# Performance work log

Hardware: AMD Instinct MI355X
Metric: run time of the kernel (lower is better)

Reference implementation:

```python
import jax, jax.numpy as jnp
import numpy as np

EPS = 1e-12  # torch F.normalize eps


def unfold(x, ksize, pad):
    # torch F.unfold equivalent: [B,C,H,W] -> [B, C*k*k, L], channel-major ordering
    patches = jax.lax.conv_general_dilated_patches(
        x, (ksize, ksize), (1, 1), [(pad, pad), (pad, pad)],
        dimension_numbers=('NCHW', 'OIHW', 'NCHW'))
    B, CKK, Hp, Wp = patches.shape
    return patches.reshape(B, CKK, Hp * Wp)


def fold(patches, C, ksize, H, W, pad):
    # torch F.fold equivalent (stride 1): overlap-add of [B, C*k*k, H*W] -> [B,C,H,W]
    B = patches.shape[0]
    p = patches.reshape(B, C, ksize, ksize, H, W)
    out = jnp.zeros((B, C, H + 2 * pad, W + 2 * pad), patches.dtype)
    for di in range(ksize):
        for dj in range(ksize):
            out = out.at[:, :, di:di + H, dj:dj + W].add(p[:, :, di, dj])
    return out[:, :, pad:pad + H, pad:pad + W]


def setup_inputs() -> dict:
    key = jax.random.key(0)
    ks = jax.random.split(key, 4)
    B, C, H, W = 2, 512, 64, 64
    D, CIN = 256, 512 * 9  # embed: Linear(tdim*8*3*3 -> tdim*4), tdim=64
    return {
        'query': jax.random.normal(ks[0], (B, C, H, W), dtype=jnp.float32),
        'key': jax.random.normal(ks[1], (B, C, H, W), dtype=jnp.float32),
        'value': jax.random.normal(ks[2], (B, C, H, W), dtype=jnp.float32),
        'W_embed': jax.random.normal(ks[3], (D, CIN), dtype=jnp.float32) * 0.02,
        'k': 3,
    }


def reference(query, key, value, W_embed, k):
    B, Cv, H, W = value.shape
    # patch embed: unfold -> linear (no bias)
    q_unf = unfold(query, k, k // 2)                       # [B, C*k*k, L]
    k_unf = unfold(key, k, k // 2)                         # [B, C*k*k, L]
    k_emb = jnp.einsum('bcl,dc->bld', k_unf, W_embed)      # [B, L, D]
    q_emb = jnp.einsum('bcl,dc->bdl', q_unf, W_embed)      # [B, D, L]
    # cosine correlation
    k_n = k_emb / jnp.maximum(jnp.linalg.norm(k_emb, axis=2, keepdims=True), EPS)
    q_n = q_emb / jnp.maximum(jnp.linalg.norm(q_emb, axis=1, keepdims=True), EPS)
    corr = jnp.einsum('bld,bdm->blm', k_n, q_n)            # [B, L_key, L_query]
    corr_value = jnp.max(corr, axis=1)                     # [B, L]
    corr_argmax = jnp.argmax(corr, axis=1)                 # [B, L]
    # swap(V=value, idx=corr_argmax, s=1, k=k)
    s = 1
    temph = s * k + H * s - H - s                          # = k - 1
    tempw = s * k + W * s - W - s
    ph = max(temph // 2 + temph % 2, 1)
    pw = max(tempw // 2 + tempw % 2, 1)
    v_unf = unfold(value, k, ph)                           # [B, Cv*k*k, L] (ph==pw for square)
    t_unf = jnp.take_along_axis(v_unf, corr_argmax[:, None, :], axis=2)
    divisor = fold(jnp.ones_like(t_unf), Cv, k, H, W, ph)
    T = fold(t_unf, Cv, k, H, W, ph) / divisor             # [B, Cv, H, W]
    S = corr_value.reshape(B, 1, H, W)
    return S, T
```

## Files before the change

### kernel.cpp

```cpp
#include <hip/hip_runtime.h>
#include <hip/hip_bf16.h>
#include <stdint.h>
#include <math.h>

#define BB 2
#define CC 512
#define HH 64
#define WW 64
#define LL 4096
#define DD 256
#define CIN 4608
#define NT 144

typedef _Float16 half_t;
typedef __attribute__((ext_vector_type(8))) _Float16 f16x8;
typedef __attribute__((ext_vector_type(4))) _Float16 f16x4;
typedef __attribute__((ext_vector_type(4))) float f32x4;

__global__ __launch_bounds__(256) void splitW2(const float* __restrict__ W,
                                               char* __restrict__ Wst) {
    int i = blockIdx.x * 256 + threadIdx.x;
    if (i >= NT * DD * 4) return;
    int it = i >> 10;
    int r  = i & 1023;
    int d  = r >> 2;
    int fs = r & 3;
    const float* src = W + (size_t)d * CIN + it * 32 + fs * 8;
    f16x8 h8, l8;
#pragma unroll
    for (int j = 0; j < 8; j++) {
        float w = src[j];
        half_t h = (half_t)w;
        h8[j] = h;
        l8[j] = (half_t)(w - (float)h);
    }
    size_t base = (size_t)it * 32768 + d * 128;
    int sw = (d & 7) << 4;
    *(f16x8*)(Wst + base + ((fs * 16) ^ sw)) = h8;
    *(f16x8*)(Wst + base + ((64 + fs * 16) ^ sw)) = l8;
}

__device__ __forceinline__ half_t* ldsAddr(half_t* base, int r, int slot) {
    return base + r * 64 + ((slot ^ (r & 7)) << 3);
}

#define GATE4() do { asm volatile("s_waitcnt vmcnt(4) lgkmcnt(0)" ::: "memory"); \
                     __builtin_amdgcn_s_barrier(); \
                     __builtin_amdgcn_sched_barrier(0); } while (0)
#define GATE0() do { asm volatile("s_waitcnt vmcnt(0) lgkmcnt(0)" ::: "memory"); \
                     __builtin_amdgcn_s_barrier(); \
                     __builtin_amdgcn_sched_barrier(0); } while (0)

__global__ __launch_bounds__(512, 1) void embed_mfma(const float* __restrict__ query,
                                                     const float* __restrict__ key,
                                                     const char* __restrict__ Wst,
                                                     char* __restrict__ qemb,
                                                     char* __restrict__ kemb) {
    __shared__ half_t sW[2][16384];
    __shared__ half_t sB[2][4096];
    __shared__ float red[4][64];
    __shared__ float invn[64];

    int iid = blockIdx.y;
    int b = iid & 1, type = iid >> 1;
    const char* imgB = (const char*)((type ? key : query) + (size_t)b * CC * LL);
    int y  = blockIdx.x;
    int l0 = y * 64;
    int t = threadIdx.x;
    int w = t >> 6;
    int lane = t & 63;
    int wr = w >> 1;
    int wc = w & 1;
    int fr = lane & 15;
    int fs = lane >> 4;

    int xB = t & 63;
    int kcB = __builtin_amdgcn_readfirstlane(t >> 6);
    int cS = (kcB * 4) / 9;
    int offS = (kcB * 4) % 9;

    int row0 = (y > 0 ? y - 1 : 0) * 256;  int vy0 = (y > 0);
    int row1 = y * 256;
    int row2 = (y < 63 ? y + 1 : 63) * 256; int vy2 = (y < 63);
    int X0 = (xB > 0 ? xB - 1 : 0) * 4;    int vx0 = (xB > 0);
    int X1 = xB * 4;
    int X2 = (xB < 63 ? xB + 1 : 63) * 4;  int vx2 = (xB < 63);

    f32x4 acc[4][2];
#pragma unroll
    for (int rg = 0; rg < 4; rg++)
#pragma unroll
        for (int cg = 0; cg < 2; cg++) acc[rg][cg] = (f32x4){0.f, 0.f, 0.f, 0.f};

    float Bv[4];

#define LOADB()                                                          \
    do {                                                                 \
        int cj = cS, oj = offS;                                          \
        _Pragma("unroll")                                                \
        for (int j = 0; j < 4; j++) {                                    \
            int di = (oj >= 6) ? 2 : (oj >= 3) ? 1 : 0;                  \
            int dj = oj - di * 3;                                        \
            int rowb = (di == 0) ? row0 : (di == 1) ? row1 : row2;       \
            int vy   = (di == 0) ? vy0 : (di == 1) ? 1 : vy2;            \
            int xoff = (dj == 0) ? X0 : (dj == 1) ? X1 : X2;             \
            int vx   = (dj == 0) ? vx0 : (dj == 1) ? 1 : vx2;            \
            float v = *(const float*)(imgB + (((size_t)cj) << 14) + rowb + xoff); \
            Bv[j] = (vy & vx) ? v : 0.f;                                 \
            oj++; if (oj >= 9) { oj = 0; cj++; }                         \
        }                                                                \
        cS += 3; offS += 5; if (offS >= 9) { offS -= 9; cS++; }          \
    } while (0)

#define WRITEB(buf)                                                      \
    do {                                                                 \
        f16x4 h4, l4;                                                    \
        _Pragma("unroll")                                                \
        for (int j = 0; j < 4; j++) {                                    \
            half_t h = (half_t)Bv[j];                                    \
            h4[j] = h; l4[j] = (half_t)(Bv[j] - (float)h);               \
        }                                                                \
        *(f16x4*)(ldsAddr(buf, xB, kcB >> 1) + ((kcB & 1) << 2)) = h4;   \
        *(f16x4*)(ldsAddr(buf, xB, 4 + (kcB >> 1)) + ((kcB & 1) << 2)) = l4; \
    } while (0)

#define DMAW(swbuf, itv)                                                 \
    do {                                                                 \
        const char* gsrc_ = Wst + (size_t)(itv) * 32768 + t * 16;        \
        char* ldst_ = (char*)(swbuf) + t * 16;                           \
        _Pragma("unroll")                                                \
        for (int c = 0; c < 4; c++)                                      \
            __builtin_amdgcn_global_load_lds(                            \
                (const __attribute__((address_space(1))) void*)(gsrc_ + c * 8192), \
                (__attribute__((address_space(3))) void*)(ldst_ + c * 8192), 16, 0, 0); \
    } while (0)

#define READA(swbuf)                                                     \
    do {                                                                 \
        _Pragma("unroll")                                                \
        for (int rg = 0; rg < 4; rg++) {                                 \
            int dl = wr * 64 + rg * 16 + fr;                             \
            int sw_ = (dl & 7) << 4;                                     \
            const char* rowp = (const char*)(swbuf) + dl * 128;          \
            ah[rg] = *(const f16x8*)(rowp + ((fs * 16) ^ sw_));          \
            al[rg] = *(const f16x8*)(rowp + ((64 + fs * 16) ^ sw_));     \
        }                                                                \
    } while (0)

#define READB(buf)                                                       \
    do {                                                                 \
        _Pragma("unroll")                                                \
        for (int cg = 0; cg < 2; cg++) {                                 \
            int r = wc * 32 + cg * 16 + fr;                              \
            bh[cg] = *(f16x8*)ldsAddr(buf, r, fs);                       \
            bl[cg] = *(f16x8*)ldsAddr(buf, r, fs + 4);                   \
        }                                                                \
    } while (0)

#define DOMFMA()                                                         \
    do {                                                                 \
        _Pragma("unroll")                                                \
        for (int rg = 0; rg < 4; rg++)                                   \
            _Pragma("unroll")                                            \
            for (int cg = 0; cg < 2; cg++)                               \
                acc[rg][cg] = __builtin_amdgcn_mfma_f32_16x16x32_f16(ah[rg], bh[cg], acc[rg][cg], 0, 0, 0); \
        _Pragma("unroll")                                                \
        for (int rg = 0; rg < 4; rg++)                                   \
            _Pragma("unroll")                                            \
            for (int cg = 0; cg < 2; cg++) {                             \
                acc[rg][cg] = __builtin_amdgcn_mfma_f32_16x16x32_f16(ah[rg], bl[cg], acc[rg][cg], 0, 0, 0); \
                acc[rg][cg] = __builtin_amdgcn_mfma_f32_16x16x32_f16(al[rg], bh[cg], acc[rg][cg], 0, 0, 0); \
            }                                                            \
    } while (0)

    f16x8 ah[4], al[4], bh[2], bl[2];

    LOADB();
    DMAW(&sW[0][0], 0);
    __builtin_amdgcn_sched_barrier(0);
    WRITEB(&sB[0][0]);
    __builtin_amdgcn_sched_barrier(0);
    LOADB();

    half_t* swc = &sW[0][0]; half_t* swn = &sW[1][0];
    half_t* sbc = &sB[0][0]; half_t* sbn = &sB[1][0];

    for (int it = 0; it < NT - 1; ++it) {
        GATE4();
        READA(swc);
        READB(sbc);
        WRITEB(sbn);
        __builtin_amdgcn_sched_barrier(0);
        DMAW(swn, it + 1);
        __builtin_amdgcn_sched_barrier(0);
        if (it < NT - 2) LOADB();
        DOMFMA();
        half_t* tp = swc; swc = swn; swn = tp;
        tp = sbc; sbc = sbn; sbn = tp;
    }
    GATE0();
    READA(swc);
    READB(sbc);
    DOMFMA();

    float ss[2] = {0.f, 0.f};
#pragma unroll
    for (int rg = 0; rg < 4; rg++)
#pragma unroll
        for (int cg = 0; cg < 2; cg++)
#pragma unroll
            for (int r = 0; r < 4; r++) ss[cg] += acc[rg][cg][r] * acc[rg][cg][r];
#pragma unroll
    for (int cg = 0; cg < 2; cg++) {
        ss[cg] += __shfl_xor(ss[cg], 16);
        ss[cg] += __shfl_xor(ss[cg], 32);
    }
    if (lane < 16) {
        red[wr][wc * 32 + lane] = ss[0];
        red[wr][wc * 32 + 16 + lane] = ss[1];
    }
    __syncthreads();
    if (t < 64) {
        float s = red[0][t] + red[1][t] + red[2][t] + red[3][t];
        invn[t] = 1.0f / fmaxf(sqrtf(s), 1e-12f);
    }
    __syncthreads();

    char* e = (type == 0) ? qemb : kemb;
#pragma unroll
    for (int cg = 0; cg < 2; cg++) {
        int lloc = wc * 32 + cg * 16 + fr;
        float sc = invn[lloc];
        int l = l0 + lloc;
        char* rowp = e + ((size_t)b * LL + l) * 1024;
        int swb = (l & 7) << 4;
#pragma unroll
        for (int rg = 0; rg < 4; rg++) {
            int d0 = wr * 64 + rg * 16 + fs * 4;
            f16x4 h4, l4;
#pragma unroll
            for (int r = 0; r < 4; r++) {
                float v = acc[rg][cg][r] * sc;
                half_t h = (half_t)v;
                h4[r] = h;
                l4[r] = (half_t)(v - (float)h);
            }
            int itb = d0 >> 5;
            int fsc = (d0 >> 3) & 3;
            int sub = (d0 & 7) * 2;
            *(f16x4*)(rowp + itb * 128 + ((fsc * 16) ^ swb) + sub) = h4;
            *(f16x4*)(rowp + itb * 128 + ((64 + fsc * 16) ^ swb) + sub) = l4;
        }
    }
#undef LOADB
#undef WRITEB
#undef DMAW
#undef READA
#undef READB
#undef DOMFMA
}

__global__ void init_packed(unsigned long long* p, int n) {
    int i = blockIdx.x * 256 + threadIdx.x;
    if (i < n) p[i] = 0ull;
}

__global__ __launch_bounds__(256, 2) void corr_max_mfma(const char* __restrict__ kemb,
                                                        const char* __restrict__ qemb,
                                                        unsigned long long* __restrict__ packed) {
    __shared__ char sA[2][16384];
    __shared__ char sBq[2][16384];

    int b  = blockIdx.z;
    int l0 = blockIdx.y * 128;
    int m0 = blockIdx.x * 128;
    int t  = threadIdx.x;
    int w = t >> 6, lane = t & 63;
    int wr = w >> 1, wc = w & 1;
    int fr = lane & 15, fs = lane >> 4;

    const char* Abase = kemb + ((size_t)b * LL + l0) * 1024;
    const char* Bbase = qemb + ((size_t)b * LL + m0) * 1024;

    f32x4 acc[4][4];
#pragma unroll
    for (int i = 0; i < 4; i++)
#pragma unroll
        for (int j = 0; j < 4; j++) acc[i][j] = (f32x4){0.f, 0.f, 0.f, 0.f};

#define DMA2(bufi, itv)                                                   \
    do {                                                                  \
        _Pragma("unroll")                                                 \
        for (int c = 0; c < 4; c++) {                                     \
            int idx = c * 4096 + t * 16;                                  \
            int row = idx >> 7, offb = idx & 127;                         \
            __builtin_amdgcn_global_load_lds(                             \
                (const __attribute__((address_space(1))) void*)(Abase + (size_t)row * 1024 + (itv) * 128 + offb), \
                (__attribute__((address_space(3))) void*)(&sA[bufi][idx]), 16, 0, 0); \
        }                                                                 \
        _Pragma("unroll")                                                 \
        for (int c = 0; c < 4; c++) {                                     \
            int idx = c * 4096 + t * 16;                                  \
            int row = idx >> 7, offb = idx & 127;                         \
            __builtin_amdgcn_global_load_lds(                             \
                (const __attribute__((address_space(1))) void*)(Bbase + (size_t)row * 1024 + (itv) * 128 + offb), \
                (__attribute__((address_space(3))) void*)(&sBq[bufi][idx]), 16, 0, 0); \
        }                                                                 \
    } while (0)

    DMA2(0, 0);

    f16x8 ah[4], al[4], bh[4], bl[4];
    for (int it = 0; it < 8; ++it) {
        asm volatile("s_waitcnt vmcnt(0) lgkmcnt(0)" ::: "memory");
        __builtin_amdgcn_s_barrier();
        __builtin_amdgcn_sched_barrier(0);
        if (it < 7) DMA2((it + 1) & 1, it + 1);
        __builtin_amdgcn_sched_barrier(0);
        const char* sa = sA[it & 1];
        const char* sb = sBq[it & 1];
#pragma unroll
        for (int rg = 0; rg < 4; rg++) {
            int r = wr * 64 + rg * 16 + fr;
            const char* rp = sa + r * 128;
            int sw_ = (r & 7) << 4;
            ah[rg] = *(const f16x8*)(rp + ((fs * 16) ^ sw_));
            al[rg] = *(const f16x8*)(rp + ((64 + fs * 16) ^ sw_));
        }
#pragma unroll
        for (int cg = 0; cg < 4; cg++) {
            int r = wc * 64 + cg * 16 + fr;
            const char* rp = sb + r * 128;
            int sw_ = (r & 7) << 4;
            bh[cg] = *(const f16x8*)(rp + ((fs * 16) ^ sw_));
            bl[cg] = *(const f16x8*)(rp + ((64 + fs * 16) ^ sw_));
        }
#pragma unroll
        for (int rg = 0; rg < 4; rg++)
#pragma unroll
            for (int cg = 0; cg < 4; cg++)
                acc[rg][cg] = __builtin_amdgcn_mfma_f32_16x16x32_f16(ah[rg], bh[cg], acc[rg][cg], 0, 0, 0);
#pragma unroll
        for (int rg = 0; rg < 4; rg++)
#pragma unroll
            for (int cg = 0; cg < 4; cg++) {
                acc[rg][cg] = __builtin_amdgcn_mfma_f32_16x16x32_f16(ah[rg], bl[cg], acc[rg][cg], 0, 0, 0);
                acc[rg][cg] = __builtin_amdgcn_mfma_f32_16x16x32_f16(al[rg], bh[cg], acc[rg][cg], 0, 0, 0);
            }
    }
#undef DMA2

#pragma unroll
    for (int cg = 0; cg < 4; cg++) {
        unsigned long long best = 0ull;
#pragma unroll
        for (int rg = 0; rg < 4; rg++) {
#pragma unroll
            for (int r = 0; r < 4; r++) {
                unsigned u = __float_as_uint(acc[rg][cg][r]);
                u = (u & 0x80000000u) ? ~u : (u | 0x80000000u);
                int l = l0 + wr * 64 + rg * 16 + fs * 4 + r;
                unsigned long long p = ((unsigned long long)u << 32) | (unsigned)(4095 - l);
                best = (p > best) ? p : best;
            }
        }
        unsigned long long o;
        o = __shfl_xor(best, 16); best = (o > best) ? o : best;
        o = __shfl_xor(best, 32); best = (o > best) ? o : best;
        if (lane < 16)
            atomicMax(&packed[(size_t)b * LL + m0 + wc * 64 + cg * 16 + lane], best);
    }
}

__global__ void decode_packed(const unsigned long long* __restrict__ packed,
                              float* __restrict__ S_out, int* __restrict__ arg) {
    int i = blockIdx.x * 256 + threadIdx.x;
    if (i < BB * LL) {
        unsigned long long p = packed[i];
        unsigned u = (unsigned)(p >> 32);
        unsigned bits = (u & 0x80000000u) ? (u & 0x7FFFFFFFu) : ~u;
        S_out[i] = __uint_as_float(bits);
        arg[i] = 4095 - (int)(unsigned)(p & 0xFFFFFFFFull);
    }
}

__global__ __launch_bounds__(256) void transpose_mat(const float* __restrict__ src,
                                                     float* __restrict__ dst,
                                                     int R, int Cc) {
    __shared__ float tile[32][33];
    size_t boff = (size_t)blockIdx.z * R * Cc;
    int bx = blockIdx.x;
    int by = blockIdx.y;
    int tx = threadIdx.x & 31;
    int ty = threadIdx.x >> 5;
    const float* s = src + boff;
    float* d = dst + boff;
#pragma unroll
    for (int i = 0; i < 4; i++) {
        int r = by * 32 + ty + i * 8;
        int c = bx * 32 + tx;
        tile[ty + i * 8][tx] = s[(size_t)r * Cc + c];
    }
    __syncthreads();
#pragma unroll
    for (int i = 0; i < 4; i++) {
        int c = bx * 32 + ty + i * 8;
        int r = by * 32 + tx;
        d[(size_t)c * R + r] = tile[tx][ty + i * 8];
    }
}

__global__ __launch_bounds__(256) void gather_fold(const float* __restrict__ value_t,
                                                   const int* __restrict__ arg,
                                                   float* __restrict__ T_t) {
    int b = blockIdx.y;
    int pix = blockIdx.x;
    int y = pix >> 6, x = pix & 63;
    int t = threadIdx.x;
    float2 acc = make_float2(0.f, 0.f);
    int cnty = (y == 0 || y == HH - 1) ? 2 : 3;
    int cntx = (x == 0 || x == WW - 1) ? 2 : 3;
    const int* ab = arg + b * LL;
    const float* vb = value_t + (size_t)b * LL * CC;
#pragma unroll
    for (int di = 0; di < 3; di++) {
        int my = y + 1 - di;
        if (my < 0 || my >= HH) continue;
#pragma unroll
        for (int dj = 0; dj < 3; dj++) {
            int mx = x + 1 - dj;
            if (mx < 0 || mx >= WW) continue;
            int a = ab[my * WW + mx];
            int ay = a >> 6, ax = a & 63;
            int vy = ay + di - 1, vx = ax + dj - 1;
            if (vy < 0 || vy >= HH || vx < 0 || vx >= WW) continue;
            float2 v = *(const float2*)&vb[((size_t)(vy * WW + vx)) * CC + t * 2];
            acc.x += v.x; acc.y += v.y;
        }
    }
    float inv = 1.0f / (float)(cnty * cntx);
    acc.x *= inv; acc.y *= inv;
    *(float2*)&T_t[((size_t)b * LL + pix) * CC + t * 2] = acc;
}

extern "C" void kernel_launch(void* const* d_in, const int* in_sizes, int n_in,
                              void* d_out, int out_size, void* d_ws, size_t ws_size,
                              hipStream_t stream) {
    const float* query = (const float*)d_in[0];
    const float* key   = (const float*)d_in[1];
    const float* value = (const float*)d_in[2];
    const float* Wemb  = (const float*)d_in[3];

    float* out   = (float*)d_out;
    float* S_out = out;
    float* T_out = out + BB * LL;

    char* ws = (char*)d_ws;
    size_t off = 0;
    char* Wst  = ws + off; off += (size_t)NT * 32768;
    char* qemb = ws + off; off += (size_t)BB * LL * 1024;
    char* kemb = ws + off; off += (size_t)BB * LL * 1024;
    float* val_t = (float*)(ws + off); off += (size_t)BB * LL * CC * 4;
    unsigned long long* packed = (unsigned long long*)(ws + off); off += (size_t)BB * LL * 8;
    int* arg = (int*)(ws + off); off += (size_t)BB * LL * 4;
    float* T_t = (float*)ws;

    splitW2       <<<dim3(576), 256, 0, stream>>>(Wemb, Wst);
    embed_mfma    <<<dim3(64, 4), 512, 0, stream>>>(query, key, Wst, qemb, kemb);
    init_packed   <<<dim3(32), 256, 0, stream>>>(packed, BB * LL);
    corr_max_mfma <<<dim3(32, 32, 2), 256, 0, stream>>>(kemb, qemb, packed);
    decode_packed <<<dim3(32), 256, 0, stream>>>(packed, S_out, arg);
    transpose_mat <<<dim3(128, 16, 2), 256, 0, stream>>>(value, val_t, CC, LL);
    gather_fold   <<<dim3(4096, 2), 256, 0, stream>>>(val_t, arg, T_t);
    transpose_mat <<<dim3(16, 128, 2), 256, 0, stream>>>(T_t, T_out, LL, CC);
}
```

Measured before the change: 258.3 us.

## Pre-split images to fp16 hi/lo and DMA embed B-tiles into LDS

Adds a presplit kernel that transposes query/key images to pixel-major fp16 hi/lo swizzled tiles. The embed GEMM then loads a 3-row halo window per 32-channel chunk straight into LDS with global_load_lds, with a zero page for padding. It reuses that window across the 9 kernel offsets, and the weights are reordered per (channel chunk, offset) group to match. This removes the per-element scalar fp32 gather and in-kernel hi/lo conversion from the embed loop. The cost is an extra pass over the images, a larger LDS footprint and more workspace.

After: 229.3 us. 11.2% less time.

```diff
diff --git a/kernel.cpp b/kernel.cpp
--- a/kernel.cpp
+++ b/kernel.cpp
@@ -10,81 +10,174 @@
 #define LL 4096
 #define DD 256
 #define CIN 4608
-#define NT 144
+#define NG 144
 
 typedef _Float16 half_t;
 typedef __attribute__((ext_vector_type(8))) _Float16 f16x8;
 typedef __attribute__((ext_vector_type(4))) _Float16 f16x4;
 typedef __attribute__((ext_vector_type(4))) float f32x4;
 
-__global__ __launch_bounds__(256) void splitW2(const float* __restrict__ W,
-                                               char* __restrict__ Wst) {
+__global__ __launch_bounds__(256) void presplit(const float* __restrict__ query,
+                                                const float* __restrict__ key,
+                                                char* __restrict__ img_ts) {
+    __shared__ float tile[32][65];
+    int img = blockIdx.y;
+    int y   = blockIdx.x;
+    const float* src = ((img >> 1) ? key : query) + (size_t)(img & 1) * CC * LL + y * WW;
+    char* dstbase = img_ts + ((size_t)img * 64 + y) * (16 * 64 * 128);
+    int t = threadIdx.x;
+    int xl = t & 63, c4 = t >> 6;
+    int xw = t >> 2, fsw = t & 3;
+    for (int cc = 0; cc < 16; ++cc) {
+#pragma unroll
+        for (int j = 0; j < 8; ++j) {
+            int cl = c4 + j * 4;
+            tile[cl][xl] = src[(size_t)(cc * 32 + cl) * LL + xl];
+        }
+        __syncthreads();
+        f16x8 h8, l8;
+#pragma unroll
+        for (int j = 0; j < 8; ++j) {
+            float v = tile[fsw * 8 + j][xw];
+            half_t h = (half_t)v;
+            h8[j] = h; l8[j] = (half_t)(v - (float)h);
+        }
+        char* p = dstbase + (size_t)cc * 8192 + xw * 128;
+        int swz = (xw & 7) << 4;
+        *(f16x8*)(p + ((fsw * 16) ^ swz)) = h8;
+        *(f16x8*)(p + ((64 + fsw * 16) ^ swz)) = l8;
+        __syncthreads();
+    }
+}
+
+__global__ __launch_bounds__(256) void splitW2b(const float* __restrict__ W,
+                                                char* __restrict__ Wst) {
     int i = blockIdx.x * 256 + threadIdx.x;
-    if (i >= NT * DD * 4) return;
-    int it = i >> 10;
+    if (i >= NG * DD * 4) return;
+    int g  = i >> 10;
     int r  = i & 1023;
     int d  = r >> 2;
     int fs = r & 3;
-    const float* src = W + (size_t)d * CIN + it * 32 + fs * 8;
+    int cc = g / 9, o = g - cc * 9;
+    const float* src = W + (size_t)d * CIN;
     f16x8 h8, l8;
 #pragma unroll
     for (int j = 0; j < 8; j++) {
-        float w = src[j];
+        float w = src[(cc * 32 + fs * 8 + j) * 9 + o];
         half_t h = (half_t)w;
         h8[j] = h;
         l8[j] = (half_t)(w - (float)h);
     }
-    size_t base = (size_t)it * 32768 + d * 128;
+    size_t base = (size_t)g * 32768 + d * 128;
     int sw = (d & 7) << 4;
     *(f16x8*)(Wst + base + ((fs * 16) ^ sw)) = h8;
     *(f16x8*)(Wst + base + ((64 + fs * 16) ^ sw)) = l8;
 }
 
-__device__ __forceinline__ half_t* ldsAddr(half_t* base, int r, int slot) {
-    return base + r * 64 + ((slot ^ (r & 7)) << 3);
-}
-
-#define GATE4() do { asm volatile("s_waitcnt vmcnt(4) lgkmcnt(0)" ::: "memory"); \
-                     __builtin_amdgcn_s_barrier(); \
-                     __builtin_amdgcn_sched_barrier(0); } while (0)
-#define GATE0() do { asm volatile("s_waitcnt vmcnt(0) lgkmcnt(0)" ::: "memory"); \
-                     __builtin_amdgcn_s_barrier(); \
-                     __builtin_amdgcn_sched_barrier(0); } while (0)
-
-__global__ __launch_bounds__(512, 1) void embed_mfma(const float* __restrict__ query,
-                                                     const float* __restrict__ key,
-                                                     const char* __restrict__ Wst,
-                                                     char* __restrict__ qemb,
-                                                     char* __restrict__ kemb) {
-    __shared__ half_t sW[2][16384];
-    __shared__ half_t sB[2][4096];
+#define GATE() do { asm volatile("s_waitcnt vmcnt(0) lgkmcnt(0)" ::: "memory"); \
+                    __builtin_amdgcn_s_barrier(); \
+                    __builtin_amdgcn_sched_barrier(0); } while (0)
+
+__global__ __launch_bounds__(512) void embed_mfma(const char* __restrict__ img_ts,
+                                                  const char* __restrict__ Wst,
+                                                  const char* __restrict__ zp,
+                                                  char* __restrict__ qemb,
+                                                  char* __restrict__ kemb) {
+    __shared__ char sW[2][32768];
+    __shared__ char sB[2][32768];
     __shared__ float red[4][64];
     __shared__ float invn[64];
 
     int iid = blockIdx.y;
     int b = iid & 1, type = iid >> 1;
-    const char* imgB = (const char*)((type ? key : query) + (size_t)b * CC * LL);
-    int y  = blockIdx.x;
+    int y = blockIdx.x;
     int l0 = y * 64;
     int t = threadIdx.x;
-    int w = t >> 6;
-    int lane = t & 63;
-    int wr = w >> 1;
-    int wc = w & 1;
-    int fr = lane & 15;
-    int fs = lane >> 4;
-
-    int xB = t & 63;
-    int kcB = __builtin_amdgcn_readfirstlane(t >> 6);
-    int cS = (kcB * 4) / 9;
-    int offS = (kcB * 4) % 9;
-
-    int row0 = (y > 0 ? y - 1 : 0) * 256;  int vy0 = (y > 0);
-    int row1 = y * 256;
-    int row2 = (y < 63 ? y + 1 : 63) * 256; int vy2 = (y < 63);
-    int X0 = (xB > 0 ? xB - 1 : 0) * 4;    int vx0 = (xB > 0);
-    int X1 = xB * 4;
-    int X2 = (xB < 63 ? xB + 1 : 63) * 4;  int vx2 = (xB < 63);
+    int w = t >> 6, lane = t & 63;
+    int wr = w >> 1, wc = w & 1;
+    int fr = lane & 15, fs = lane >> 4;
+
+    const char* imgb = img_ts + (size_t)iid * (64 * 16 * 64 * 128);
+    const char *ps0, *ps1, *ps2, *ps3;
+    int pb0, pb1, pb2, pb3;
+#define PREP(c, PS, PB)                                                 \
+    {                                                                   \
+        int q = (c) * 512 + t;                                          \
+        int di = q / 528;                                               \
+        int rem = q - di * 528;                                         \
+        int xi = rem >> 3, sub = rem & 7;                               \
+        int xg = xi - 1, yg = y + di - 1;                               \
+        bool ok = (di < 3) && (yg >= 0) && (yg < 64) && (xg >= 0) && (xg < 64); \
+        PS = ok ? imgb + (size_t)yg * 131072 + (size_t)xg * 128 + (sub * 16) \
+                : zp + ((q & 255) * 16);                                \
+        PB = ok ? 8192 : 0;                                             \
+    }
+    PREP(0, ps0, pb0); PREP(1, ps1, pb1); PREP(2, ps2, pb2); PREP(3, ps3, pb3);
+
+    const char* pW = Wst;
+
+#define DMAW(dst)                                                       \
+    do {                                                                \
+        _Pragma("unroll")                                               \
+        for (int c = 0; c < 4; c++)                                     \
+            __builtin_amdgcn_global_load_lds(                           \
+                (const __attribute__((address_space(1))) void*)(pW + c * 8192 + t * 16), \
+                (__attribute__((address_space(3))) void*)((dst) + c * 8192 + t * 16), 16, 0, 0); \
+        pW += 32768;                                                    \
+    } while (0)
+
+#define DMAB(dst)                                                       \
+    do {                                                                \
+        __builtin_amdgcn_global_load_lds((const __attribute__((address_space(1))) void*)ps0, \
+            (__attribute__((address_space(3))) void*)((dst) + t * 16), 16, 0, 0); \
+        __builtin_amdgcn_global_load_lds((const __attribute__((address_space(1))) void*)ps1, \
+            (__attribute__((address_space(3))) void*)((dst) + 8192 + t * 16), 16, 0, 0); \
+        __builtin_amdgcn_global_load_lds((const __attribute__((address_space(1))) void*)ps2, \
+            (__attribute__((address_space(3))) void*)((dst) + 16384 + t * 16), 16, 0, 0); \
+        __builtin_amdgcn_global_load_lds((const __attribute__((address_space(1))) void*)ps3, \
+            (__attribute__((address_space(3))) void*)((dst) + 24576 + t * 16), 16, 0, 0); \
+        ps0 += pb0; ps1 += pb1; ps2 += pb2; ps3 += pb3;                 \
+    } while (0)
+
+#define READA(AH, AL, wbuf)                                             \
+    do {                                                                \
+        _Pragma("unroll")                                               \
+        for (int rg = 0; rg < 4; rg++) {                                \
+            int dl = wr * 64 + rg * 16 + fr;                            \
+            int sw_ = (dl & 7) << 4;                                    \
+            const char* rowp = (const char*)(wbuf) + dl * 128;          \
+            AH[rg] = *(const f16x8*)(rowp + ((fs * 16) ^ sw_));         \
+            AL[rg] = *(const f16x8*)(rowp + ((64 + fs * 16) ^ sw_));    \
+        }                                                               \
+    } while (0)
+
+#define READB(BH, BL, bbuf, di_, dj_)                                   \
+    do {                                                                \
+        _Pragma("unroll")                                               \
+        for (int cg = 0; cg < 2; cg++) {                                \
+            int xi = wc * 32 + cg * 16 + fr + (dj_);                    \
+            int sw_ = ((xi - 1) & 7) << 4;                              \
+            const char* rowp = (const char*)(bbuf) + (di_) * 8448 + xi * 128; \
+            BH[cg] = *(const f16x8*)(rowp + ((fs * 16) ^ sw_));         \
+            BL[cg] = *(const f16x8*)(rowp + ((64 + fs * 16) ^ sw_));    \
+        }                                                               \
+    } while (0)
+
+#define DOMFMA(AH, AL, BH, BL)                                          \
+    do {                                                                \
+        _Pragma("unroll")                                               \
+        for (int rg = 0; rg < 4; rg++)                                  \
+            _Pragma("unroll")                                           \
+            for (int cg = 0; cg < 2; cg++)                              \
+                acc[rg][cg] = __builtin_amdgcn_mfma_f32_16x16x32_f16(AH[rg], BH[cg], acc[rg][cg], 0, 0, 0); \
+        _Pragma("unroll")                                               \
+        for (int rg = 0; rg < 4; rg++)                                  \
+            _Pragma("unroll")                                           \
+            for (int cg = 0; cg < 2; cg++) {                            \
+                acc[rg][cg] = __builtin_amdgcn_mfma_f32_16x16x32_f16(AH[rg], BL[cg], acc[rg][cg], 0, 0, 0); \
+                acc[rg][cg] = __builtin_amdgcn_mfma_f32_16x16x32_f16(AL[rg], BH[cg], acc[rg][cg], 0, 0, 0); \
+            }                                                           \
+    } while (0)
 
     f32x4 acc[4][2];
 #pragma unroll
@@ -92,116 +185,55 @@
 #pragma unroll
         for (int cg = 0; cg < 2; cg++) acc[rg][cg] = (f32x4){0.f, 0.f, 0.f, 0.f};
 
-    float Bv[4];
-
-#define LOADB()                                                          \
-    do {                                                                 \
-        int cj = cS, oj = offS;                                          \
-        _Pragma("unroll")                                                \
-        for (int j = 0; j < 4; j++) {                                    \
-            int di = (oj >= 6) ? 2 : (oj >= 3) ? 1 : 0;                  \
-            int dj = oj - di * 3;                                        \
-            int rowb = (di == 0) ? row0 : (di == 1) ? row1 : row2;       \
-            int vy   = (di == 0) ? vy0 : (di == 1) ? 1 : vy2;            \
-            int xoff = (dj == 0) ? X0 : (dj == 1) ? X1 : X2;             \
-            int vx   = (dj == 0) ? vx0 : (dj == 1) ? 1 : vx2;            \
-            float v = *(const float*)(imgB + (((size_t)cj) << 14) + rowb + xoff); \
-            Bv[j] = (vy & vx) ? v : 0.f;                                 \
-            oj++; if (oj >= 9) { oj = 0; cj++; }                         \
-        }                                                                \
-        cS += 3; offS += 5; if (offS >= 9) { offS -= 9; cS++; }          \
-    } while (0)
-
-#define WRITEB(buf)                                                      \
-    do {                                                                 \
-        f16x4 h4, l4;                                                    \
-        _Pragma("unroll")                                                \
-        for (int j = 0; j < 4; j++) {                                    \
-            half_t h = (half_t)Bv[j];                                    \
-            h4[j] = h; l4[j] = (half_t)(Bv[j] - (float)h);               \
-        }                                                                \
-        *(f16x4*)(ldsAddr(buf, xB, kcB >> 1) + ((kcB & 1) << 2)) = h4;   \
-        *(f16x4*)(ldsAddr(buf, xB, 4 + (kcB >> 1)) + ((kcB & 1) << 2)) = l4; \
-    } while (0)
-
-#define DMAW(swbuf, itv)                                                 \
-    do {                                                                 \
-        const char* gsrc_ = Wst + (size_t)(itv) * 32768 + t * 16;        \
-        char* ldst_ = (char*)(swbuf) + t * 16;                           \
-        _Pragma("unroll")                                                \
-        for (int c = 0; c < 4; c++)                                      \
-            __builtin_amdgcn_global_load_lds(                            \
-                (const __attribute__((address_space(1))) void*)(gsrc_ + c * 8192), \
-                (__attribute__((address_space(3))) void*)(ldst_ + c * 8192), 16, 0, 0); \
-    } while (0)
-
-#define READA(swbuf)                                                     \
-    do {                                                                 \
-        _Pragma("unroll")                                                \
-        for (int rg = 0; rg < 4; rg++) {                                 \
-            int dl = wr * 64 + rg * 16 + fr;                             \
-            int sw_ = (dl & 7) << 4;                                     \
-            const char* rowp = (const char*)(swbuf) + dl * 128;          \
-            ah[rg] = *(const f16x8*)(rowp + ((fs * 16) ^ sw_));          \
-            al[rg] = *(const f16x8*)(rowp + ((64 + fs * 16) ^ sw_));     \
-        }                                                                \
-    } while (0)
-
-#define READB(buf)                                                       \
-    do {                                                                 \
-        _Pragma("unroll")                                                \
-        for (int cg = 0; cg < 2; cg++) {                                 \
-            int r = wc * 32 + cg * 16 + fr;                              \
-            bh[cg] = *(f16x8*)ldsAddr(buf, r, fs);                       \
-            bl[cg] = *(f16x8*)ldsAddr(buf, r, fs + 4);                   \
-        }                                                                \
-    } while (0)
-
-#define DOMFMA()                                                         \
-    do {                                                                 \
-        _Pragma("unroll")                                                \
-        for (int rg = 0; rg < 4; rg++)                                   \
-            _Pragma("unroll")                                            \
-            for (int cg = 0; cg < 2; cg++)                               \
-                acc[rg][cg] = __builtin_amdgcn_mfma_f32_16x16x32_f16(ah[rg], bh[cg], acc[rg][cg], 0, 0, 0); \
-        _Pragma("unroll")                                                \
-        for (int rg = 0; rg < 4; rg++)                                   \
-            _Pragma("unroll")                                            \
-            for (int cg = 0; cg < 2; cg++) {                             \
-                acc[rg][cg] = __builtin_amdgcn_mfma_f32_16x16x32_f16(ah[rg], bl[cg], acc[rg][cg], 0, 0, 0); \
-                acc[rg][cg] = __builtin_amdgcn_mfma_f32_16x16x32_f16(al[rg], bh[cg], acc[rg][cg], 0, 0, 0); \
-            }                                                            \
-    } while (0)
-
-    f16x8 ah[4], al[4], bh[2], bl[2];
-
-    LOADB();
-    DMAW(&sW[0][0], 0);
+    f16x8 ah0[4], al0[4], bh0[2], bl0[2];
+    f16x8 ah1[4], al1[4], bh1[2], bl1[2];
+
+    char* wb0 = &sW[0][0]; char* wb1 = &sW[1][0];
+    char* b0 = &sB[0][0];  char* b1 = &sB[1][0];
+
+    DMAB(b0);
+    DMAW(wb0);
+    GATE();
+    READA(ah0, al0, wb0);
+    READB(bh0, bl0, b0, 0, 0);
+    DMAW(wb1);
+    DMAB(b1);
     __builtin_amdgcn_sched_barrier(0);
-    WRITEB(&sB[0][0]);
+
+    int o = 1, issued = 2;
+    char* bcur = b0;
+    char* bnext = b0;
+
+#define HALF(AHr, ALr, BHr, BLr, WRD, WWR, AHm, ALm, BHm, BLm)          \
+    GATE();                                                             \
+    READA(AHr, ALr, WRD);                                               \
+    {                                                                   \
+        int di_ = (o >= 6) ? 2 : (o >= 3) ? 1 : 0;                      \
+        int dj_ = o - di_ * 3;                                          \
+        READB(BHr, BLr, bcur, di_, dj_);                                \
+    }                                                                   \
+    DMAW(WWR);                                                          \
+    if (o == 0 && issued < 16) {                                        \
+        DMAB(bnext);                                                    \
+        bnext = (bnext == b0) ? b1 : b0;                                \
+        issued++;                                                       \
+    }                                                                   \
+    o++; if (o == 9) { o = 0; bcur = (bcur == b0) ? b1 : b0; }          \
+    __builtin_amdgcn_sched_barrier(0);                                  \
+    DOMFMA(AHm, ALm, BHm, BLm);
+
+#pragma unroll 1
+    for (int i = 0; i < 71; ++i) {
+        HALF(ah1, al1, bh1, bl1, wb1, wb0, ah0, al0, bh0, bl0)
+        HALF(ah0, al0, bh0, bl0, wb0, wb1, ah1, al1, bh1, bl1)
+    }
+    GATE();
+    READA(ah1, al1, wb1);
+    READB(bh1, bl1, bcur, 2, 2);
     __builtin_amdgcn_sched_barrier(0);
-    LOADB();
-
-    half_t* swc = &sW[0][0]; half_t* swn = &sW[1][0];
-    half_t* sbc = &sB[0][0]; half_t* sbn = &sB[1][0];
-
-    for (int it = 0; it < NT - 1; ++it) {
-        GATE4();
-        READA(swc);
-        READB(sbc);
-        WRITEB(sbn);
-        __builtin_amdgcn_sched_barrier(0);
-        DMAW(swn, it + 1);
-        __builtin_amdgcn_sched_barrier(0);
-        if (it < NT - 2) LOADB();
-        DOMFMA();
-        half_t* tp = swc; swc = swn; swn = tp;
-        tp = sbc; sbc = sbn; sbn = tp;
-    }
-    GATE0();
-    READA(swc);
-    READB(sbc);
-    DOMFMA();
+    DOMFMA(ah0, al0, bh0, bl0);
+    DOMFMA(ah1, al1, bh1, bl1);
+#undef HALF
 
     float ss[2] = {0.f, 0.f};
 #pragma unroll
@@ -252,9 +284,9 @@
             *(f16x4*)(rowp + itb * 128 + ((64 + fsc * 16) ^ swb) + sub) = l4;
         }
     }
-#undef LOADB
-#undef WRITEB
+#undef PREP
 #undef DMAW
+#undef DMAB
 #undef READA
 #undef READB
 #undef DOMFMA
@@ -364,9 +396,9 @@
                 best = (p > best) ? p : best;
             }
         }
-        unsigned long long o;
-        o = __shfl_xor(best, 16); best = (o > best) ? o : best;
-        o = __shfl_xor(best, 32); best = (o > best) ? o : best;
+        unsigned long long oo;
+        oo = __shfl_xor(best, 16); best = (oo > best) ? oo : best;
+        oo = __shfl_xor(best, 32); best = (oo > best) ? oo : best;
         if (lane < 16)
             atomicMax(&packed[(size_t)b * LL + m0 + wc * 64 + cg * 16 + lane], best);
     }
@@ -456,18 +488,20 @@
     float* T_out = out + BB * LL;
 
     char* ws = (char*)d_ws;
-    size_t off = 0;
-    char* Wst  = ws + off; off += (size_t)NT * 32768;
-    char* qemb = ws + off; off += (size_t)BB * LL * 1024;
-    char* kemb = ws + off; off += (size_t)BB * LL * 1024;
-    float* val_t = (float*)(ws + off); off += (size_t)BB * LL * CC * 4;
-    unsigned long long* packed = (unsigned long long*)(ws + off); off += (size_t)BB * LL * 8;
-    int* arg = (int*)(ws + off); off += (size_t)BB * LL * 4;
-    float* T_t = (float*)ws;
-
-    splitW2       <<<dim3(576), 256, 0, stream>>>(Wemb, Wst);
-    embed_mfma    <<<dim3(64, 4), 512, 0, stream>>>(query, key, Wst, qemb, kemb);
-    init_packed   <<<dim3(32), 256, 0, stream>>>(packed, BB * LL);
+    char* img_ts = ws;
+    char* Wst    = ws + 33554432;
+    char* qemb   = ws + 38273024;
+    char* kemb   = ws + 46661632;
+    unsigned long long* packed = (unsigned long long*)(ws + 55050240);
+    char* zp     = ws + 55115776;
+    int*  arg    = (int*)(ws + 55119872);
+    float* val_t = (float*)ws;
+    float* T_t   = (float*)(ws + 16777216);
+
+    init_packed   <<<dim3(34), 256, 0, stream>>>(packed, 8704);
+    presplit      <<<dim3(64, 4), 256, 0, stream>>>(query, key, img_ts);
+    splitW2b      <<<dim3(576), 256, 0, stream>>>(Wemb, Wst);
+    embed_mfma    <<<dim3(64, 4), 512, 0, stream>>>(img_ts, Wst, zp, qemb, kemb);
     corr_max_mfma <<<dim3(32, 32, 2), 256, 0, stream>>>(kemb, qemb, packed);
     decode_packed <<<dim3(32), 256, 0, stream>>>(packed, S_out, arg);
     transpose_mat <<<dim3(128, 16, 2), 256, 0, stream>>>(value, val_t, CC, LL);
```
